# Kernel optimization log

Hardware: AMD Instinct MI355X
Metric: run time of the kernel (lower is better)

## Reference

```python
import jax, jax.numpy as jnp
import numpy as np

NQ, NL, QD, LD, H = 100000, 32, 384, 1024, 128
E, E_SEE, E_PRED = 1000000, 750000, 250000
N = NQ + NL
EPS = 1e-5


def _bn(x, g, b):
    # BatchNorm1d in training mode: biased batch statistics over node dim
    mu = x.mean(0)
    var = x.var(0)
    return g * (x - mu) * jax.lax.rsqrt(var + EPS) + b


def _general_conv(x, src, dst, ea, Wm, bm, We, be_):
    # PyG GeneralConv (heads=1, no attention, aggr='add', in==out -> identity skip)
    msg = x[src] @ Wm + bm + ea @ We + be_            # [E_see, H]
    agg = jax.ops.segment_sum(msg, dst, num_segments=N)
    return agg + x


def setup_inputs() -> dict:
    key = jax.random.key(0)
    ks = jax.random.split(key, 20)
    s = lambda fan_in: 1.0 / np.sqrt(fan_in)
    return {
        'query_features': jax.random.normal(ks[0], (NQ, QD), jnp.float32),
        'llm_features': jax.random.normal(ks[1], (NL, LD), jnp.float32),
        'edge_index': jax.random.randint(ks[2], (2, E), 0, N, jnp.int64 if jax.config.jax_enable_x64 else jnp.int32),
        'edge_mask': jax.random.randint(ks[3], (E_PRED,), 0, E),
        'edge_can_see': jax.random.randint(ks[4], (E_SEE,), 0, E),
        'edge_weight': jax.random.uniform(ks[5], (E, 1), jnp.float32),
        'Wq': jax.random.normal(ks[6], (QD, H), jnp.float32) * s(QD),
        'bq': jnp.zeros((H,), jnp.float32),
        'Wl': jax.random.normal(ks[7], (LD, H), jnp.float32) * s(LD),
        'bl': jnp.zeros((H,), jnp.float32),
        'W_em': jax.random.normal(ks[8], (1, 1), jnp.float32),
        'b_em': jnp.zeros((1,), jnp.float32),
        'W1m': jax.random.normal(ks[9], (H, H), jnp.float32) * s(H),
        'b1m': jnp.zeros((H,), jnp.float32),
        'W1e': jax.random.normal(ks[10], (1, H), jnp.float32),
        'b1e': jnp.zeros((H,), jnp.float32),
        'W2m': jax.random.normal(ks[11], (H, H), jnp.float32) * s(H),
        'b2m': jnp.zeros((H,), jnp.float32),
        'W2e': jax.random.normal(ks[12], (1, H), jnp.float32),
        'b2e': jnp.zeros((H,), jnp.float32),
        'g1': jnp.ones((H,), jnp.float32), 'beta1': jnp.zeros((H,), jnp.float32),
        'g2': jnp.ones((H,), jnp.float32), 'beta2': jnp.zeros((H,), jnp.float32),
    }


def reference(query_features, llm_features, edge_index, edge_mask, edge_can_see,
              edge_weight, Wq, bq, Wl, bl, W_em, b_em, W1m, b1m, W1e, b1e,
              W2m, b2m, W2e, b2e, g1, beta1, g2, beta2):
    lrelu = jax.nn.leaky_relu  # slope 0.01 (torch default)
    ei_mask = edge_index[:, edge_can_see]       # [2, E_see]
    ei_pred = edge_index[:, edge_mask]          # [2, E_pred]
    ew = lrelu(edge_weight[edge_can_see] @ W_em + b_em)  # [E_see, 1]
    # feature alignment
    x_ini = jnp.concatenate([query_features @ Wq + bq, llm_features @ Wl + bl], 0)  # [N, H]
    src, dst = ei_mask[0], ei_mask[1]
    x = lrelu(_bn(_general_conv(x_ini, src, dst, ew, W1m, b1m, W1e, b1e), g1, beta1))
    x = _bn(_general_conv(x, src, dst, ew, W2m, b2m, W2e, b2e), g2, beta2)
    edge_predict = jax.nn.sigmoid((x_ini[ei_pred[0]] * x[ei_pred[1]]).mean(-1))  # [E_pred]
    return edge_predict
```

## Files before the change

kernel.cpp:

```cpp
#include <hip/hip_runtime.h>
#include <math.h>

#define NQ 100000
#define NL 32
#define QD 384
#define LD 1024
#define H 128
#define E_TOT 1000000
#define E_SEE 750000
#define E_PRED 250000
#define NN (NQ + NL)
#define EPS 1e-5f

#define NB_SCAN ((NN + 255) / 256)
#define NB_GEMM ((NN + 127) / 128)
#define NB_XINI ((NQ + 127) / 128)

typedef __attribute__((ext_vector_type(8))) short short8;
typedef __attribute__((ext_vector_type(4))) short short4v;
typedef __attribute__((ext_vector_type(4))) float f32x4;

__device__ __forceinline__ unsigned short f2bf(float f) {
  unsigned int u = __builtin_bit_cast(unsigned int, f);
  u = (u + 0x7FFFu + ((u >> 16) & 1u)) >> 16;
  return (unsigned short)u;
}


__global__ void k_ew_hist(const int* __restrict__ ecs, const int* __restrict__ EI,
                          const float* __restrict__ ewt, const float* __restrict__ Wem,
                          const float* __restrict__ bem, float* __restrict__ ew,
                          int* __restrict__ cnt) {
  int e = blockIdx.x * 256 + threadIdx.x;
  if (e >= E_SEE) return;
  int idx = ecs[e];
  int d = EI[E_TOT + idx];
  atomicAdd(&cnt[d], 1);
  float w = ewt[idx] * Wem[0] + bem[0];
  ew[e] = w > 0.f ? w : 0.01f * w;
}

__global__ void k_scan_block(const int* __restrict__ cnt, int* __restrict__ bsum) {
  __shared__ int red[256];
  int i = blockIdx.x * 256 + threadIdx.x;
  red[threadIdx.x] = (i < NN) ? cnt[i] : 0;
  __syncthreads();
  for (int s = 128; s > 0; s >>= 1) {
    if (threadIdx.x < s) red[threadIdx.x] += red[threadIdx.x + s];
    __syncthreads();
  }
  if (threadIdx.x == 0) bsum[blockIdx.x] = red[0];
}

__global__ void k_scan_top(const int* __restrict__ bsum, int* __restrict__ boff) {
  __shared__ int buf[2][512];
  int t = threadIdx.x;
  int v = (t < NB_SCAN) ? bsum[t] : 0;
  buf[0][t] = v;
  __syncthreads();
  int src = 0;
  for (int d = 1; d < 512; d <<= 1) {
    int x = buf[src][t];
    if (t >= d) x += buf[src][t - d];
    buf[src ^ 1][t] = x;
    __syncthreads();
    src ^= 1;
  }
  if (t < NB_SCAN) boff[t] = buf[src][t] - v;
}

__global__ void k_scan_write(const int* __restrict__ cnt, const int* __restrict__ boff,
                             int* __restrict__ off) {
  __shared__ int buf[2][256];
  int t = threadIdx.x;
  int i = blockIdx.x * 256 + t;
  int v = (i < NN) ? cnt[i] : 0;
  buf[0][t] = v;
  __syncthreads();
  int src = 0;
  for (int d = 1; d < 256; d <<= 1) {
    int x = buf[src][t];
    if (t >= d) x += buf[src][t - d];
    buf[src ^ 1][t] = x;
    __syncthreads();
    src ^= 1;
  }
  if (i < NN) off[i] = boff[blockIdx.x] + buf[src][t] - v;
  if (i == 0) off[NN] = E_SEE;
}

__global__ void k_fill(const int* __restrict__ ecs, const int* __restrict__ EI,
                       const float* __restrict__ ew, const int* __restrict__ off,
                       int* __restrict__ cur, int* __restrict__ csr_src,
                       float* __restrict__ csr_ew) {
  int e = blockIdx.x * 256 + threadIdx.x;
  if (e >= E_SEE) return;
  int idx = ecs[e];
  int s = EI[idx];
  int d = EI[E_TOT + idx];
  int p = off[d] + atomicAdd(&cur[d], 1);
  csr_src[p] = s;
  csr_ew[p] = ew[e];
}


__global__ void k_prep(const float* __restrict__ Wq, const float* __restrict__ W1m,
                       const float* __restrict__ W2m,
                       unsigned short* __restrict__ Wqt, unsigned short* __restrict__ W1t,
                       unsigned short* __restrict__ W2t) {
  int i = blockIdx.x * 256 + threadIdx.x;
  const int tot1 = QD * H;
  const int tot2 = H * H;
  if (i < tot1) {
    int n = i / QD, k = i - n * QD;
    Wqt[i] = f2bf(Wq[(size_t)k * H + n]);
  } else if (i < tot1 + tot2) {
    int j = i - tot1;
    int n = j >> 7, k = j & 127;
    W1t[j] = f2bf(W1m[(size_t)k * H + n]);
  } else if (i < tot1 + 2 * tot2) {
    int j = i - tot1 - tot2;
    int n = j >> 7, k = j & 127;
    W2t[j] = f2bf(W2m[(size_t)k * H + n]);
  }
}


__global__ __launch_bounds__(128) void k_llm_part(const float* __restrict__ lf,
                                                  const float* __restrict__ Wl,
                                                  float* __restrict__ part) {
  int r = blockIdx.x >> 3;
  int s = blockIdx.x & 7;
  int t = threadIdx.x;
  int k0 = s * 128;
  float acc = 0.f;
#pragma unroll 4
  for (int k = 0; k < 128; k += 4) {
    float a0 = lf[(size_t)r * LD + k0 + k + 0];
    float a1 = lf[(size_t)r * LD + k0 + k + 1];
    float a2 = lf[(size_t)r * LD + k0 + k + 2];
    float a3 = lf[(size_t)r * LD + k0 + k + 3];
    acc = fmaf(a0, Wl[(size_t)(k0 + k + 0) * H + t], acc);
    acc = fmaf(a1, Wl[(size_t)(k0 + k + 1) * H + t], acc);
    acc = fmaf(a2, Wl[(size_t)(k0 + k + 2) * H + t], acc);
    acc = fmaf(a3, Wl[(size_t)(k0 + k + 3) * H + t], acc);
  }
  part[(size_t)blockIdx.x * 128 + t] = acc;
}

__global__ void k_llm_comb(const float* __restrict__ part, const float* __restrict__ bl,
                           float* __restrict__ XINI) {
  int i = blockIdx.x * 256 + threadIdx.x;
  if (i >= NL * H) return;
  int r = i >> 7, t = i & 127;
  float a = bl[t];
#pragma unroll
  for (int s = 0; s < 8; s++) a += part[(size_t)(r * 8 + s) * 128 + t];
  XINI[(size_t)(NQ + r) * H + t] = a;
}


__global__ __launch_bounds__(256) void k_xini(
    const float* __restrict__ qf, const unsigned short* __restrict__ Wqt,
    const float* __restrict__ bq, float* __restrict__ XINI) {
  __shared__ unsigned short sA[128][40];
  __shared__ unsigned short sB[128][40];
  int tid = threadIdx.x;
  int w = tid >> 6, lane = tid & 63;
  int l15 = lane & 15, quad = lane >> 4;
  int wr = (w >> 1) * 64, wc = (w & 1) * 64;
  int rowbase = blockIdx.x * 128;
  f32x4 acc[4][4];
#pragma unroll
  for (int i = 0; i < 4; i++)
#pragma unroll
    for (int j = 0; j < 4; j++) acc[i][j] = (f32x4){0.f, 0.f, 0.f, 0.f};

  int arow = tid >> 3, akc = (tid & 7) * 4;
  int bn = tid >> 2, bk8 = (tid & 3) * 8;
  float4 pa[4];
  int4 pb[2];
#pragma unroll
  for (int p = 0; p < 4; ++p) {
    int gr = rowbase + p * 32 + arow;
    pa[p] = (gr < NQ) ? *(const float4*)&qf[(size_t)gr * QD + akc]
                      : make_float4(0.f, 0.f, 0.f, 0.f);
  }
#pragma unroll
  for (int p = 0; p < 2; ++p)
    pb[p] = *(const int4*)&Wqt[(size_t)(p * 64 + bn) * QD + bk8];

  for (int step = 0; step < 12; ++step) {
    int kb = step * 32;
#pragma unroll
    for (int p = 0; p < 4; ++p) {
      short4v b;
      b.x = (short)f2bf(pa[p].x); b.y = (short)f2bf(pa[p].y);
      b.z = (short)f2bf(pa[p].z); b.w = (short)f2bf(pa[p].w);
      *(short4v*)&sA[p * 32 + arow][akc] = b;
    }
#pragma unroll
    for (int p = 0; p < 2; ++p) *(int4*)&sB[p * 64 + bn][bk8] = pb[p];
    __syncthreads();
    if (step + 1 < 12) {
      int kn = kb + 32;
#pragma unroll
      for (int p = 0; p < 4; ++p) {
        int gr = rowbase + p * 32 + arow;
        pa[p] = (gr < NQ) ? *(const float4*)&qf[(size_t)gr * QD + kn + akc]
                          : make_float4(0.f, 0.f, 0.f, 0.f);
      }
#pragma unroll
      for (int p = 0; p < 2; ++p)
        pb[p] = *(const int4*)&Wqt[(size_t)(p * 64 + bn) * QD + kn + bk8];
    }
    short8 af[4], bfr[4];
#pragma unroll
    for (int mt = 0; mt < 4; ++mt)
      af[mt] = *(const short8*)&sA[wr + mt * 16 + l15][quad * 8];
#pragma unroll
    for (int nt = 0; nt < 4; ++nt)
      bfr[nt] = *(const short8*)&sB[wc + nt * 16 + l15][quad * 8];
#pragma unroll
    for (int mt = 0; mt < 4; ++mt)
#pragma unroll
      for (int nt = 0; nt < 4; ++nt)
        acc[mt][nt] = __builtin_amdgcn_mfma_f32_16x16x32_bf16(
            af[mt], bfr[nt], acc[mt][nt], 0, 0, 0);
    __syncthreads();
  }
#pragma unroll
  for (int nt = 0; nt < 4; ++nt) {
    int col = wc + nt * 16 + l15;
    float bias = bq[col];
#pragma unroll
    for (int mt = 0; mt < 4; ++mt) {
#pragma unroll
      for (int r = 0; r < 4; ++r) {
        int n = rowbase + wr + mt * 16 + quad * 4 + r;
        if (n < NQ) XINI[(size_t)n * H + col] = acc[mt][nt][r] + bias;
      }
    }
  }
}


template <bool TRANS>
__global__ __launch_bounds__(256) void k_seg(
    const float* __restrict__ Xin, const int* __restrict__ off,
    const int* __restrict__ csr_src, const float* __restrict__ csr_ew,
    const float* __restrict__ scale, const float* __restrict__ shift,
    unsigned short* __restrict__ S16, float* __restrict__ swsum,
    float* __restrict__ degf) {
  int w = blockIdx.x * 4 + (threadIdx.x >> 6);
  if (w >= NN) return;
  int lane = threadIdx.x & 63;
  int o0 = off[w], o1 = off[w + 1];
  float ax = 1.f, ay = 1.f, bx = 0.f, by = 0.f;
  if (TRANS) {
    float2 sc = *(const float2*)&scale[lane * 2];
    float2 sh = *(const float2*)&shift[lane * 2];
    ax = sc.x; ay = sc.y; bx = sh.x; by = sh.y;
  }
  float accx = 0.f, accy = 0.f, ews = 0.f;
  for (int k = o0; k < o1; ++k) {
    int s = csr_src[k];
    float2 v = *(const float2*)&Xin[(size_t)s * H + lane * 2];
    if (TRANS) {
      float t0 = fmaf(ax, v.x, bx); v.x = t0 > 0.f ? t0 : 0.01f * t0;
      float t1 = fmaf(ay, v.y, by); v.y = t1 > 0.f ? t1 : 0.01f * t1;
    }
    accx += v.x; accy += v.y;
    ews += csr_ew[k];
  }
  unsigned int pk = ((unsigned int)f2bf(accy) << 16) | f2bf(accx);
  *(unsigned int*)&S16[(size_t)w * H + lane * 2] = pk;
  if (lane == 0) { swsum[w] = ews; degf[w] = (float)(o1 - o0); }
}


template <bool TRANS>
__global__ __launch_bounds__(256) void k_gemm(
    const unsigned short* __restrict__ S16, const float* __restrict__ Xin,
    float* __restrict__ Xout, const unsigned short* __restrict__ Wt,
    const float* __restrict__ bm, const float* __restrict__ be,
    const float* __restrict__ We,
    const float* __restrict__ scale, const float* __restrict__ shift,
    const float* __restrict__ swsum, const float* __restrict__ degf,
    float* __restrict__ partials) {
  __shared__ unsigned short sA[128][40];
  __shared__ unsigned short sB[128][40];
  __shared__ float st[2][8][128];
  int tid = threadIdx.x;
  int w = tid >> 6, lane = tid & 63;
  int l15 = lane & 15, quad = lane >> 4;
  int wr = (w >> 1) * 64, wc = (w & 1) * 64;
  int rowbase = blockIdx.x * 128;
  f32x4 acc[4][4];
#pragma unroll
  for (int i = 0; i < 4; i++)
#pragma unroll
    for (int j = 0; j < 4; j++) acc[i][j] = (f32x4){0.f, 0.f, 0.f, 0.f};

  int arow = tid >> 1, ah = (tid & 1) * 16;
  int4 pa[2], pb[2];
  {
    int gr = rowbase + arow;
    if (gr < NN) {
      pa[0] = *(const int4*)&S16[(size_t)gr * H + ah];
      pa[1] = *(const int4*)&S16[(size_t)gr * H + ah + 8];
    } else {
      pa[0] = make_int4(0, 0, 0, 0); pa[1] = make_int4(0, 0, 0, 0);
    }
    pb[0] = *(const int4*)&Wt[(size_t)arow * H + ah];
    pb[1] = *(const int4*)&Wt[(size_t)arow * H + ah + 8];
  }
  for (int step = 0; step < 4; ++step) {
    *(int4*)&sA[arow][ah] = pa[0];
    *(int4*)&sA[arow][ah + 8] = pa[1];
    *(int4*)&sB[arow][ah] = pb[0];
    *(int4*)&sB[arow][ah + 8] = pb[1];
    __syncthreads();
    if (step + 1 < 4) {
      int kn = (step + 1) * 32;
      int gr = rowbase + arow;
      if (gr < NN) {
        pa[0] = *(const int4*)&S16[(size_t)gr * H + kn + ah];
        pa[1] = *(const int4*)&S16[(size_t)gr * H + kn + ah + 8];
      } else {
        pa[0] = make_int4(0, 0, 0, 0); pa[1] = make_int4(0, 0, 0, 0);
      }
      pb[0] = *(const int4*)&Wt[(size_t)arow * H + kn + ah];
      pb[1] = *(const int4*)&Wt[(size_t)arow * H + kn + ah + 8];
    }
    short8 af[4], bfr[4];
#pragma unroll
    for (int mt = 0; mt < 4; ++mt)
      af[mt] = *(const short8*)&sA[wr + mt * 16 + l15][quad * 8];
#pragma unroll
    for (int nt = 0; nt < 4; ++nt)
      bfr[nt] = *(const short8*)&sB[wc + nt * 16 + l15][quad * 8];
#pragma unroll
    for (int mt = 0; mt < 4; ++mt)
#pragma unroll
      for (int nt = 0; nt < 4; ++nt)
        acc[mt][nt] = __builtin_amdgcn_mfma_f32_16x16x32_bf16(
            af[mt], bfr[nt], acc[mt][nt], 0, 0, 0);
    __syncthreads();
  }
  int col4[4];
  float cb4[4], we4[4], sc4[4], sh4[4], ps[4], pq[4];
#pragma unroll
  for (int nt = 0; nt < 4; ++nt) {
    int col = wc + nt * 16 + l15;
    col4[nt] = col;
    cb4[nt] = bm[col] + be[col];
    we4[nt] = We[col];
    if (TRANS) { sc4[nt] = scale[col]; sh4[nt] = shift[col]; }
    ps[nt] = 0.f; pq[nt] = 0.f;
  }
#pragma unroll
  for (int mt = 0; mt < 4; ++mt) {
#pragma unroll
    for (int r = 0; r < 4; ++r) {
      int n = rowbase + wr + mt * 16 + quad * 4 + r;
      if (n < NN) {
        float dg = degf[n], sw = swsum[n];
#pragma unroll
        for (int nt = 0; nt < 4; ++nt) {
          float rr = Xin[(size_t)n * H + col4[nt]];
          if (TRANS) {
            float t = fmaf(sc4[nt], rr, sh4[nt]);
            rr = t > 0.f ? t : 0.01f * t;
          }
          float o = acc[mt][nt][r] + dg * cb4[nt] + sw * we4[nt] + rr;
          Xout[(size_t)n * H + col4[nt]] = o;
          ps[nt] += o; pq[nt] += o * o;
        }
      }
    }
  }
  int slot = (w >> 1) * 4 + quad;
#pragma unroll
  for (int nt = 0; nt < 4; ++nt) {
    st[0][slot][col4[nt]] = ps[nt];
    st[1][slot][col4[nt]] = pq[nt];
  }
  __syncthreads();
  int plane = tid >> 7, col = tid & 127;
  float s = 0.f;
#pragma unroll
  for (int y = 0; y < 8; y++) s += st[plane][y][col];
  partials[(size_t)blockIdx.x * 256 + tid] = s;
}


__global__ __launch_bounds__(256) void k_bnstats(
    const float* __restrict__ partials, const float* __restrict__ g,
    const float* __restrict__ beta, float* __restrict__ scale,
    float* __restrict__ shift) {
  __shared__ float rs[256], rq[256];
  int j = blockIdx.x;
  int t = threadIdx.x;
  float as = 0.f, aq = 0.f;
  for (int b = t; b < NB_GEMM; b += 256) {
    as += partials[(size_t)b * 256 + j];
    aq += partials[(size_t)b * 256 + 128 + j];
  }
  rs[t] = as; rq[t] = aq;
  __syncthreads();
  for (int s = 128; s > 0; s >>= 1) {
    if (t < s) { rs[t] += rs[t + s]; rq[t] += rq[t + s]; }
    __syncthreads();
  }
  if (t == 0) {
    float mean = rs[0] / (float)NN;
    float var = rq[0] / (float)NN - mean * mean;
    float a = g[j] * rsqrtf(var + EPS);
    scale[j] = a;
    shift[j] = beta[j] - mean * a;
  }
}


__global__ __launch_bounds__(256) void k_pred(
    const int* __restrict__ emask, const int* __restrict__ EI,
    const float* __restrict__ XINI, const float* __restrict__ X,
    const float* __restrict__ scale, const float* __restrict__ shift,
    float* __restrict__ out) {
  int i = blockIdx.x * 4 + (threadIdx.x >> 6);
  if (i >= E_PRED) return;
  int lane = threadIdx.x & 63;
  int m = emask[i];
  int p0 = EI[m];
  int p1 = EI[E_TOT + m];
  float2 a = *(const float2*)&XINI[(size_t)p0 * H + lane * 2];
  float2 b = *(const float2*)&X[(size_t)p1 * H + lane * 2];
  float2 sc = *(const float2*)&scale[lane * 2];
  float2 sh = *(const float2*)&shift[lane * 2];
  float v = a.x * fmaf(sc.x, b.x, sh.x) + a.y * fmaf(sc.y, b.y, sh.y);
#pragma unroll
  for (int mm = 32; mm > 0; mm >>= 1) v += __shfl_xor(v, mm, 64);
  if (lane == 0) out[i] = 1.f / (1.f + expf(-v * (1.f / 128.f)));
}


extern "C" void kernel_launch(void* const* d_in, const int* in_sizes, int n_in,
                              void* d_out, int out_size, void* d_ws, size_t ws_size,
                              hipStream_t stream) {
  const float* qf    = (const float*)d_in[0];
  const float* lf    = (const float*)d_in[1];
  const int*   EI    = (const int*)d_in[2];
  const int*   emask = (const int*)d_in[3];
  const int*   ecs   = (const int*)d_in[4];
  const float* ewt   = (const float*)d_in[5];
  const float* Wq    = (const float*)d_in[6];
  const float* bq    = (const float*)d_in[7];
  const float* Wl    = (const float*)d_in[8];
  const float* bl    = (const float*)d_in[9];
  const float* Wem   = (const float*)d_in[10];
  const float* bem   = (const float*)d_in[11];
  const float* W1m   = (const float*)d_in[12];
  const float* b1m   = (const float*)d_in[13];
  const float* W1e   = (const float*)d_in[14];
  const float* b1e   = (const float*)d_in[15];
  const float* W2m   = (const float*)d_in[16];
  const float* b2m   = (const float*)d_in[17];
  const float* W2e   = (const float*)d_in[18];
  const float* b2e   = (const float*)d_in[19];
  const float* g1    = (const float*)d_in[20];
  const float* beta1 = (const float*)d_in[21];
  const float* g2    = (const float*)d_in[22];
  const float* beta2 = (const float*)d_in[23];
  float* out = (float*)d_out;

  char* p = (char*)d_ws;
  auto alloc = [&](size_t bytes) -> void* {
    void* r = (void*)p;
    p += (bytes + 255) & ~(size_t)255;
    return r;
  };
  float* XINI    = (float*)alloc((size_t)NN * H * 4);
  float* X       = (float*)alloc((size_t)NN * H * 4);
  unsigned short* S16 = (unsigned short*)alloc((size_t)NN * H * 2);
  float* ew      = (float*)alloc((size_t)E_SEE * 4);
  float* csr_ew  = (float*)alloc((size_t)E_SEE * 4);
  int*   csr_src = (int*)alloc((size_t)E_SEE * 4);
  int*   cnt     = (int*)alloc((size_t)NN * 4);
  int*   off     = (int*)alloc((size_t)(NN + 1) * 4);
  int*   cur     = (int*)alloc((size_t)NN * 4);
  int*   bsum    = (int*)alloc((size_t)NB_SCAN * 4);
  int*   boff    = (int*)alloc((size_t)NB_SCAN * 4);
  float* swsum   = (float*)alloc((size_t)NN * 4);
  float* degf    = (float*)alloc((size_t)NN * 4);
  float* partials= (float*)alloc((size_t)NB_GEMM * 256 * 4);
  float* scale1  = (float*)alloc(128 * 4);
  float* shift1  = (float*)alloc(128 * 4);
  float* scale2  = (float*)alloc(128 * 4);
  float* shift2  = (float*)alloc(128 * 4);
  unsigned short* Wqt = (unsigned short*)alloc((size_t)QD * H * 2);
  unsigned short* W1t = (unsigned short*)alloc((size_t)H * H * 2);
  unsigned short* W2t = (unsigned short*)alloc((size_t)H * H * 2);
  float* llmpart = (float*)alloc((size_t)NL * 8 * H * 4);

  hipMemsetAsync(cnt, 0, (size_t)NN * 4, stream);
  hipMemsetAsync(cur, 0, (size_t)NN * 4, stream);

  int ebl = (E_SEE + 255) / 256;
  k_prep<<<320, 256, 0, stream>>>(Wq, W1m, W2m, Wqt, W1t, W2t);
  k_ew_hist<<<ebl, 256, 0, stream>>>(ecs, EI, ewt, Wem, bem, ew, cnt);
  k_scan_block<<<NB_SCAN, 256, 0, stream>>>(cnt, bsum);
  k_scan_top<<<1, 512, 0, stream>>>(bsum, boff);
  k_scan_write<<<NB_SCAN, 256, 0, stream>>>(cnt, boff, off);
  k_fill<<<ebl, 256, 0, stream>>>(ecs, EI, ew, off, cur, csr_src, csr_ew);

  k_llm_part<<<NL * 8, 128, 0, stream>>>(lf, Wl, llmpart);
  k_llm_comb<<<(NL * H + 255) / 256, 256, 0, stream>>>(llmpart, bl, XINI);
  k_xini<<<NB_XINI, 256, 0, stream>>>(qf, Wqt, bq, XINI);

  int segbl = (NN + 3) / 4;
  k_seg<false><<<segbl, 256, 0, stream>>>(XINI, off, csr_src, csr_ew,
                                          nullptr, nullptr, S16, swsum, degf);
  k_gemm<false><<<NB_GEMM, 256, 0, stream>>>(S16, XINI, X, W1t, b1m, b1e, W1e,
                                             nullptr, nullptr, swsum, degf, partials);
  k_bnstats<<<H, 256, 0, stream>>>(partials, g1, beta1, scale1, shift1);
  k_seg<true><<<segbl, 256, 0, stream>>>(X, off, csr_src, csr_ew,
                                         scale1, shift1, S16, swsum, degf);
  k_gemm<true><<<NB_GEMM, 256, 0, stream>>>(S16, X, X, W2t, b2m, b2e, W2e,
                                            scale1, shift1, swsum, degf, partials);
  k_bnstats<<<H, 256, 0, stream>>>(partials, g2, beta2, scale2, shift2);
  int pbl = (E_PRED + 3) / 4;
  k_pred<<<pbl, 256, 0, stream>>>(emask, EI, XINI, X, scale2, shift2, out);
}
```

Before: 724.5 us.

## Shrink GEMM row tiles to 64, swap MFMA operands for vectorized epilogue, cache edge endpoints

The xini and conv GEMM kernels now process 64 rows per block instead of 128. They swap the MFMA operand roles so each lane holds four consecutive output columns, which lets the epilogue use float4 loads and stores and reduce BN statistics with wave shuffles. The histogram kernel also stores the (src,dst) pair for each visible edge so the fill kernel reads it coalesced instead of re-gathering through edge_can_see and edge_index. Smaller tiles double the block count for better occupancy and load balance, but they reload the weight tile more often and add an extra int2 buffer write.

```diff
diff --git a/kernel.cpp b/kernel.cpp
--- a/kernel.cpp
+++ b/kernel.cpp
@@ -13,8 +13,8 @@
 #define EPS 1e-5f
 
 #define NB_SCAN ((NN + 255) / 256)
-#define NB_GEMM ((NN + 127) / 128)
-#define NB_XINI ((NQ + 127) / 128)
+#define NB_G64 (NN / 64)
+#define NB_X64 ((NQ + 63) / 64)
 
 typedef __attribute__((ext_vector_type(8))) short short8;
 typedef __attribute__((ext_vector_type(4))) short short4v;
@@ -30,11 +30,13 @@
 __global__ void k_ew_hist(const int* __restrict__ ecs, const int* __restrict__ EI,
                           const float* __restrict__ ewt, const float* __restrict__ Wem,
                           const float* __restrict__ bem, float* __restrict__ ew,
-                          int* __restrict__ cnt) {
+                          int* __restrict__ cnt, int2* __restrict__ se) {
   int e = blockIdx.x * 256 + threadIdx.x;
   if (e >= E_SEE) return;
   int idx = ecs[e];
+  int s = EI[idx];
   int d = EI[E_TOT + idx];
+  se[e] = make_int2(s, d);
   atomicAdd(&cnt[d], 1);
   float w = ewt[idx] * Wem[0] + bem[0];
   ew[e] = w > 0.f ? w : 0.01f * w;
@@ -89,17 +91,14 @@
   if (i == 0) off[NN] = E_SEE;
 }
 
-__global__ void k_fill(const int* __restrict__ ecs, const int* __restrict__ EI,
-                       const float* __restrict__ ew, const int* __restrict__ off,
-                       int* __restrict__ cur, int* __restrict__ csr_src,
-                       float* __restrict__ csr_ew) {
+__global__ void k_fill(const int2* __restrict__ se, const float* __restrict__ ew,
+                       const int* __restrict__ off, int* __restrict__ cur,
+                       int* __restrict__ csr_src, float* __restrict__ csr_ew) {
   int e = blockIdx.x * 256 + threadIdx.x;
   if (e >= E_SEE) return;
-  int idx = ecs[e];
-  int s = EI[idx];
-  int d = EI[E_TOT + idx];
-  int p = off[d] + atomicAdd(&cur[d], 1);
-  csr_src[p] = s;
+  int2 sd = se[e];
+  int p = off[sd.y] + atomicAdd(&cur[sd.y], 1);
+  csr_src[p] = sd.x;
   csr_ew[p] = ew[e];
 }
 
@@ -163,25 +162,26 @@
 __global__ __launch_bounds__(256) void k_xini(
     const float* __restrict__ qf, const unsigned short* __restrict__ Wqt,
     const float* __restrict__ bq, float* __restrict__ XINI) {
-  __shared__ unsigned short sA[128][40];
+  __shared__ unsigned short sA[64][40];
   __shared__ unsigned short sB[128][40];
   int tid = threadIdx.x;
   int w = tid >> 6, lane = tid & 63;
   int l15 = lane & 15, quad = lane >> 4;
-  int wr = (w >> 1) * 64, wc = (w & 1) * 64;
-  int rowbase = blockIdx.x * 128;
-  f32x4 acc[4][4];
-#pragma unroll
-  for (int i = 0; i < 4; i++)
+  int wn = (w >> 1) * 32;
+  int wm = (w & 1) * 64;
+  int rowbase = blockIdx.x * 64;
+  f32x4 acc[2][4];
+#pragma unroll
+  for (int i = 0; i < 2; i++)
 #pragma unroll
     for (int j = 0; j < 4; j++) acc[i][j] = (f32x4){0.f, 0.f, 0.f, 0.f};
 
   int arow = tid >> 3, akc = (tid & 7) * 4;
   int bn = tid >> 2, bk8 = (tid & 3) * 8;
-  float4 pa[4];
+  float4 pa[2];
   int4 pb[2];
 #pragma unroll
-  for (int p = 0; p < 4; ++p) {
+  for (int p = 0; p < 2; ++p) {
     int gr = rowbase + p * 32 + arow;
     pa[p] = (gr < NQ) ? *(const float4*)&qf[(size_t)gr * QD + akc]
                       : make_float4(0.f, 0.f, 0.f, 0.f);
@@ -191,9 +191,8 @@
     pb[p] = *(const int4*)&Wqt[(size_t)(p * 64 + bn) * QD + bk8];
 
   for (int step = 0; step < 12; ++step) {
-    int kb = step * 32;
-#pragma unroll
-    for (int p = 0; p < 4; ++p) {
+#pragma unroll
+    for (int p = 0; p < 2; ++p) {
       short4v b;
       b.x = (short)f2bf(pa[p].x); b.y = (short)f2bf(pa[p].y);
       b.z = (short)f2bf(pa[p].z); b.w = (short)f2bf(pa[p].w);
@@ -203,9 +202,9 @@
     for (int p = 0; p < 2; ++p) *(int4*)&sB[p * 64 + bn][bk8] = pb[p];
     __syncthreads();
     if (step + 1 < 12) {
-      int kn = kb + 32;
-#pragma unroll
-      for (int p = 0; p < 4; ++p) {
+      int kn = (step + 1) * 32;
+#pragma unroll
+      for (int p = 0; p < 2; ++p) {
         int gr = rowbase + p * 32 + arow;
         pa[p] = (gr < NQ) ? *(const float4*)&qf[(size_t)gr * QD + kn + akc]
                           : make_float4(0.f, 0.f, 0.f, 0.f);
@@ -214,31 +213,32 @@
       for (int p = 0; p < 2; ++p)
         pb[p] = *(const int4*)&Wqt[(size_t)(p * 64 + bn) * QD + kn + bk8];
     }
-    short8 af[4], bfr[4];
+    short8 af[4], bfr[2];
 #pragma unroll
     for (int mt = 0; mt < 4; ++mt)
-      af[mt] = *(const short8*)&sA[wr + mt * 16 + l15][quad * 8];
-#pragma unroll
-    for (int nt = 0; nt < 4; ++nt)
-      bfr[nt] = *(const short8*)&sB[wc + nt * 16 + l15][quad * 8];
-#pragma unroll
-    for (int mt = 0; mt < 4; ++mt)
-#pragma unroll
-      for (int nt = 0; nt < 4; ++nt)
-        acc[mt][nt] = __builtin_amdgcn_mfma_f32_16x16x32_bf16(
-            af[mt], bfr[nt], acc[mt][nt], 0, 0, 0);
-    __syncthreads();
-  }
-#pragma unroll
-  for (int nt = 0; nt < 4; ++nt) {
-    int col = wc + nt * 16 + l15;
-    float bias = bq[col];
-#pragma unroll
-    for (int mt = 0; mt < 4; ++mt) {
-#pragma unroll
-      for (int r = 0; r < 4; ++r) {
-        int n = rowbase + wr + mt * 16 + quad * 4 + r;
-        if (n < NQ) XINI[(size_t)n * H + col] = acc[mt][nt][r] + bias;
+      af[mt] = *(const short8*)&sB[wm + mt * 16 + l15][quad * 8];
+#pragma unroll
+    for (int nt = 0; nt < 2; ++nt)
+      bfr[nt] = *(const short8*)&sA[wn + nt * 16 + l15][quad * 8];
+#pragma unroll
+    for (int nt = 0; nt < 2; ++nt)
+#pragma unroll
+      for (int mt = 0; mt < 4; ++mt)
+        acc[nt][mt] = __builtin_amdgcn_mfma_f32_16x16x32_bf16(
+            af[mt], bfr[nt], acc[nt][mt], 0, 0, 0);
+    __syncthreads();
+  }
+#pragma unroll
+  for (int nt = 0; nt < 2; ++nt) {
+    int row = rowbase + wn + nt * 16 + l15;
+    if (row < NQ) {
+#pragma unroll
+      for (int mt = 0; mt < 4; ++mt) {
+        int cb = wm + mt * 16 + quad * 4;
+        float4 bias = *(const float4*)&bq[cb];
+        float4 o = make_float4(acc[nt][mt][0] + bias.x, acc[nt][mt][1] + bias.y,
+                               acc[nt][mt][2] + bias.z, acc[nt][mt][3] + bias.w);
+        *(float4*)&XINI[(size_t)row * H + cb] = o;
       }
     }
   }
@@ -288,110 +288,106 @@
     const float* __restrict__ scale, const float* __restrict__ shift,
     const float* __restrict__ swsum, const float* __restrict__ degf,
     float* __restrict__ partials) {
-  __shared__ unsigned short sA[128][40];
+  __shared__ unsigned short sA[64][40];
   __shared__ unsigned short sB[128][40];
-  __shared__ float st[2][8][128];
+  __shared__ float st[2][2][128];
   int tid = threadIdx.x;
   int w = tid >> 6, lane = tid & 63;
   int l15 = lane & 15, quad = lane >> 4;
-  int wr = (w >> 1) * 64, wc = (w & 1) * 64;
-  int rowbase = blockIdx.x * 128;
-  f32x4 acc[4][4];
-#pragma unroll
-  for (int i = 0; i < 4; i++)
+  int wn = (w >> 1) * 32, wm = (w & 1) * 64;
+  int rowbase = blockIdx.x * 64;
+  f32x4 acc[2][4];
+#pragma unroll
+  for (int i = 0; i < 2; i++)
 #pragma unroll
     for (int j = 0; j < 4; j++) acc[i][j] = (f32x4){0.f, 0.f, 0.f, 0.f};
 
-  int arow = tid >> 1, ah = (tid & 1) * 16;
-  int4 pa[2], pb[2];
-  {
-    int gr = rowbase + arow;
-    if (gr < NN) {
-      pa[0] = *(const int4*)&S16[(size_t)gr * H + ah];
-      pa[1] = *(const int4*)&S16[(size_t)gr * H + ah + 8];
-    } else {
-      pa[0] = make_int4(0, 0, 0, 0); pa[1] = make_int4(0, 0, 0, 0);
-    }
-    pb[0] = *(const int4*)&Wt[(size_t)arow * H + ah];
-    pb[1] = *(const int4*)&Wt[(size_t)arow * H + ah + 8];
-  }
+  int arow = tid >> 2, ak8 = (tid & 3) * 8;
+  int bn = tid >> 2, bk8 = (tid & 3) * 8;
+  int4 pa;
+  int4 pb[2];
+  pa = *(const int4*)&S16[(size_t)(rowbase + arow) * H + ak8];
+#pragma unroll
+  for (int p = 0; p < 2; ++p)
+    pb[p] = *(const int4*)&Wt[(size_t)(p * 64 + bn) * H + bk8];
+
   for (int step = 0; step < 4; ++step) {
-    *(int4*)&sA[arow][ah] = pa[0];
-    *(int4*)&sA[arow][ah + 8] = pa[1];
-    *(int4*)&sB[arow][ah] = pb[0];
-    *(int4*)&sB[arow][ah + 8] = pb[1];
+    *(int4*)&sA[arow][ak8] = pa;
+#pragma unroll
+    for (int p = 0; p < 2; ++p) *(int4*)&sB[p * 64 + bn][bk8] = pb[p];
     __syncthreads();
     if (step + 1 < 4) {
       int kn = (step + 1) * 32;
-      int gr = rowbase + arow;
-      if (gr < NN) {
-        pa[0] = *(const int4*)&S16[(size_t)gr * H + kn + ah];
-        pa[1] = *(const int4*)&S16[(size_t)gr * H + kn + ah + 8];
-      } else {
-        pa[0] = make_int4(0, 0, 0, 0); pa[1] = make_int4(0, 0, 0, 0);
+      pa = *(const int4*)&S16[(size_t)(rowbase + arow) * H + kn + ak8];
+#pragma unroll
+      for (int p = 0; p < 2; ++p)
+        pb[p] = *(const int4*)&Wt[(size_t)(p * 64 + bn) * H + kn + bk8];
+    }
+    short8 af[4], bfr[2];
+#pragma unroll
+    for (int mt = 0; mt < 4; ++mt)
+      af[mt] = *(const short8*)&sB[wm + mt * 16 + l15][quad * 8];
+#pragma unroll
+    for (int nt = 0; nt < 2; ++nt)
+      bfr[nt] = *(const short8*)&sA[wn + nt * 16 + l15][quad * 8];
+#pragma unroll
+    for (int nt = 0; nt < 2; ++nt)
+#pragma unroll
+      for (int mt = 0; mt < 4; ++mt)
+        acc[nt][mt] = __builtin_amdgcn_mfma_f32_16x16x32_bf16(
+            af[mt], bfr[nt], acc[nt][mt], 0, 0, 0);
+    __syncthreads();
+  }
+  int n0 = rowbase + wn + l15;
+  float dg0 = degf[n0], sw0 = swsum[n0];
+  float dg1 = degf[n0 + 16], sw1 = swsum[n0 + 16];
+#pragma unroll
+  for (int mt = 0; mt < 4; ++mt) {
+    int cb = wm + mt * 16 + quad * 4;
+    float4 m4 = *(const float4*)&bm[cb];
+    float4 e4 = *(const float4*)&be[cb];
+    float4 cb4 = make_float4(m4.x + e4.x, m4.y + e4.y, m4.z + e4.z, m4.w + e4.w);
+    float4 we4 = *(const float4*)&We[cb];
+    float4 sc4, sh4;
+    if (TRANS) { sc4 = *(const float4*)&scale[cb]; sh4 = *(const float4*)&shift[cb]; }
+    f32x4 psum = {0.f, 0.f, 0.f, 0.f}, psq = {0.f, 0.f, 0.f, 0.f};
+#pragma unroll
+    for (int nt = 0; nt < 2; ++nt) {
+      int n = n0 + nt * 16;
+      float dg = nt ? dg1 : dg0, sw = nt ? sw1 : sw0;
+      float4 rr = *(const float4*)&Xin[(size_t)n * H + cb];
+      if (TRANS) {
+        float t;
+        t = fmaf(sc4.x, rr.x, sh4.x); rr.x = t > 0.f ? t : 0.01f * t;
+        t = fmaf(sc4.y, rr.y, sh4.y); rr.y = t > 0.f ? t : 0.01f * t;
+        t = fmaf(sc4.z, rr.z, sh4.z); rr.z = t > 0.f ? t : 0.01f * t;
+        t = fmaf(sc4.w, rr.w, sh4.w); rr.w = t > 0.f ? t : 0.01f * t;
       }
-      pb[0] = *(const int4*)&Wt[(size_t)arow * H + kn + ah];
-      pb[1] = *(const int4*)&Wt[(size_t)arow * H + kn + ah + 8];
-    }
-    short8 af[4], bfr[4];
-#pragma unroll
-    for (int mt = 0; mt < 4; ++mt)
-      af[mt] = *(const short8*)&sA[wr + mt * 16 + l15][quad * 8];
-#pragma unroll
-    for (int nt = 0; nt < 4; ++nt)
-      bfr[nt] = *(const short8*)&sB[wc + nt * 16 + l15][quad * 8];
-#pragma unroll
-    for (int mt = 0; mt < 4; ++mt)
-#pragma unroll
-      for (int nt = 0; nt < 4; ++nt)
-        acc[mt][nt] = __builtin_amdgcn_mfma_f32_16x16x32_bf16(
-            af[mt], bfr[nt], acc[mt][nt], 0, 0, 0);
-    __syncthreads();
-  }
-  int col4[4];
-  float cb4[4], we4[4], sc4[4], sh4[4], ps[4], pq[4];
-#pragma unroll
-  for (int nt = 0; nt < 4; ++nt) {
-    int col = wc + nt * 16 + l15;
-    col4[nt] = col;
-    cb4[nt] = bm[col] + be[col];
-    we4[nt] = We[col];
-    if (TRANS) { sc4[nt] = scale[col]; sh4[nt] = shift[col]; }
-    ps[nt] = 0.f; pq[nt] = 0.f;
-  }
-#pragma unroll
-  for (int mt = 0; mt < 4; ++mt) {
-#pragma unroll
-    for (int r = 0; r < 4; ++r) {
-      int n = rowbase + wr + mt * 16 + quad * 4 + r;
-      if (n < NN) {
-        float dg = degf[n], sw = swsum[n];
-#pragma unroll
-        for (int nt = 0; nt < 4; ++nt) {
-          float rr = Xin[(size_t)n * H + col4[nt]];
-          if (TRANS) {
-            float t = fmaf(sc4[nt], rr, sh4[nt]);
-            rr = t > 0.f ? t : 0.01f * t;
-          }
-          float o = acc[mt][nt][r] + dg * cb4[nt] + sw * we4[nt] + rr;
-          Xout[(size_t)n * H + col4[nt]] = o;
-          ps[nt] += o; pq[nt] += o * o;
-        }
+      float4 o;
+      o.x = acc[nt][mt][0] + dg * cb4.x + sw * we4.x + rr.x;
+      o.y = acc[nt][mt][1] + dg * cb4.y + sw * we4.y + rr.y;
+      o.z = acc[nt][mt][2] + dg * cb4.z + sw * we4.z + rr.z;
+      o.w = acc[nt][mt][3] + dg * cb4.w + sw * we4.w + rr.w;
+      *(float4*)&Xout[(size_t)n * H + cb] = o;
+      psum[0] += o.x; psum[1] += o.y; psum[2] += o.z; psum[3] += o.w;
+      psq[0] += o.x * o.x; psq[1] += o.y * o.y; psq[2] += o.z * o.z; psq[3] += o.w * o.w;
+    }
+#pragma unroll
+    for (int s = 1; s < 16; s <<= 1) {
+#pragma unroll
+      for (int j = 0; j < 4; ++j) {
+        psum[j] += __shfl_xor(psum[j], s, 64);
+        psq[j] += __shfl_xor(psq[j], s, 64);
       }
     }
-  }
-  int slot = (w >> 1) * 4 + quad;
-#pragma unroll
-  for (int nt = 0; nt < 4; ++nt) {
-    st[0][slot][col4[nt]] = ps[nt];
-    st[1][slot][col4[nt]] = pq[nt];
+    if (l15 == 0) {
+      *(f32x4*)&st[0][w >> 1][cb] = psum;
+      *(f32x4*)&st[1][w >> 1][cb] = psq;
+    }
   }
   __syncthreads();
-  int plane = tid >> 7, col = tid & 127;
-  float s = 0.f;
-#pragma unroll
-  for (int y = 0; y < 8; y++) s += st[plane][y][col];
-  partials[(size_t)blockIdx.x * 256 + tid] = s;
+  int stat = tid >> 7, col = tid & 127;
+  partials[(size_t)blockIdx.x * 256 + tid] = st[stat][0][col] + st[stat][1][col];
 }
 
 
@@ -403,7 +399,7 @@
   int j = blockIdx.x;
   int t = threadIdx.x;
   float as = 0.f, aq = 0.f;
-  for (int b = t; b < NB_GEMM; b += 256) {
+  for (int b = t; b < NB_G64; b += 256) {
     as += partials[(size_t)b * 256 + j];
     aq += partials[(size_t)b * 256 + 128 + j];
   }
@@ -486,6 +482,7 @@
   float* ew      = (float*)alloc((size_t)E_SEE * 4);
   float* csr_ew  = (float*)alloc((size_t)E_SEE * 4);
   int*   csr_src = (int*)alloc((size_t)E_SEE * 4);
+  int2*  se      = (int2*)alloc((size_t)E_SEE * 8);
   int*   cnt     = (int*)alloc((size_t)NN * 4);
   int*   off     = (int*)alloc((size_t)(NN + 1) * 4);
   int*   cur     = (int*)alloc((size_t)NN * 4);
@@ -493,7 +490,7 @@
   int*   boff    = (int*)alloc((size_t)NB_SCAN * 4);
   float* swsum   = (float*)alloc((size_t)NN * 4);
   float* degf    = (float*)alloc((size_t)NN * 4);
-  float* partials= (float*)alloc((size_t)NB_GEMM * 256 * 4);
+  float* partials= (float*)alloc((size_t)NB_G64 * 256 * 4);
   float* scale1  = (float*)alloc(128 * 4);
   float* shift1  = (float*)alloc(128 * 4);
   float* scale2  = (float*)alloc(128 * 4);
@@ -508,26 +505,26 @@
 
   int ebl = (E_SEE + 255) / 256;
   k_prep<<<320, 256, 0, stream>>>(Wq, W1m, W2m, Wqt, W1t, W2t);
-  k_ew_hist<<<ebl, 256, 0, stream>>>(ecs, EI, ewt, Wem, bem, ew, cnt);
+  k_ew_hist<<<ebl, 256, 0, stream>>>(ecs, EI, ewt, Wem, bem, ew, cnt, se);
   k_scan_block<<<NB_SCAN, 256, 0, stream>>>(cnt, bsum);
   k_scan_top<<<1, 512, 0, stream>>>(bsum, boff);
   k_scan_write<<<NB_SCAN, 256, 0, stream>>>(cnt, boff, off);
-  k_fill<<<ebl, 256, 0, stream>>>(ecs, EI, ew, off, cur, csr_src, csr_ew);
+  k_fill<<<ebl, 256, 0, stream>>>(se, ew, off, cur, csr_src, csr_ew);
 
   k_llm_part<<<NL * 8, 128, 0, stream>>>(lf, Wl, llmpart);
   k_llm_comb<<<(NL * H + 255) / 256, 256, 0, stream>>>(llmpart, bl, XINI);
-  k_xini<<<NB_XINI, 256, 0, stream>>>(qf, Wqt, bq, XINI);
+  k_xini<<<NB_X64, 256, 0, stream>>>(qf, Wqt, bq, XINI);
 
   int segbl = (NN + 3) / 4;
   k_seg<false><<<segbl, 256, 0, stream>>>(XINI, off, csr_src, csr_ew,
                                           nullptr, nullptr, S16, swsum, degf);
-  k_gemm<false><<<NB_GEMM, 256, 0, stream>>>(S16, XINI, X, W1t, b1m, b1e, W1e,
-                                             nullptr, nullptr, swsum, degf, partials);
+  k_gemm<false><<<NB_G64, 256, 0, stream>>>(S16, XINI, X, W1t, b1m, b1e, W1e,
+                                            nullptr, nullptr, swsum, degf, partials);
   k_bnstats<<<H, 256, 0, stream>>>(partials, g1, beta1, scale1, shift1);
   k_seg<true><<<segbl, 256, 0, stream>>>(X, off, csr_src, csr_ew,
                                          scale1, shift1, S16, swsum, degf);
-  k_gemm<true><<<NB_GEMM, 256, 0, stream>>>(S16, X, X, W2t, b2m, b2e, W2e,
-                                            scale1, shift1, swsum, degf, partials);
+  k_gemm<true><<<NB_G64, 256, 0, stream>>>(S16, X, X, W2t, b2m, b2e, W2e,
+                                           scale1, shift1, swsum, degf, partials);
   k_bnstats<<<H, 256, 0, stream>>>(partials, g2, beta2, scale2, shift2);
   int pbl = (E_PRED + 3) / 4;
   k_pred<<<pbl, 256, 0, stream>>>(emask, EI, XINI, X, scale2, shift2, out);
```

New measurement: 736.1 us. Within noise of the previous version (+1.6%).
